# Performance work log

Measured on AMD Instinct MI355X. Metric: run time of the kernel, lower is better.

The kernel has to match this reference:

```python
import jax, jax.numpy as jnp
import numpy as np

N_NODES = 50000
N_EDGES = 800000
D = 128
N_LAYERS = 6  # nbaselayer=3 -> branches of depth 1,2,3
NBASELAYER = 3
BN_EPS = 1e-5


def setup_inputs() -> dict:
    key = jax.random.key(0)
    ks = jax.random.split(key, 11)
    stdv = 1.0 / np.sqrt(D)
    return {
        "x": jax.random.normal(ks[0], (N_NODES, D), jnp.float32),
        "row": jax.random.randint(ks[1], (N_EDGES,), 0, N_NODES),
        "col": jax.random.randint(ks[2], (N_EDGES,), 0, N_NODES),
        "edge_weight": jax.random.uniform(ks[3], (N_EDGES,), jnp.float32),
        "W": jax.random.uniform(ks[4], (N_LAYERS, D, D), jnp.float32, -stdv, stdv),
        "SW": jax.random.uniform(ks[5], (N_LAYERS, D, D), jnp.float32, -stdv, stdv),
        "b": jax.random.uniform(ks[6], (N_LAYERS, D), jnp.float32, -stdv, stdv),
        "gamma": jax.random.uniform(ks[7], (N_LAYERS, D), jnp.float32, 0.5, 1.5),
        "beta": jax.random.normal(ks[8], (N_LAYERS, D), jnp.float32) * 0.1,
        "rmean": jax.random.normal(ks[9], (N_LAYERS, D), jnp.float32) * 0.1,
        "rvar": jax.random.uniform(ks[10], (N_LAYERS, D), jnp.float32, 0.5, 1.5),
    }


def reference(x, row, col, edge_weight, W, SW, b, gamma, beta, rmean, rvar):
    n = x.shape[0]

    def gcn(l, h):
        # dense GEMM: [N, D] @ [D, D]
        support = h @ W[l]
        # sparse aggregation (spmm): out[row] += w * support[col]
        msg = support[col] * edge_weight[:, None]  # [E, D]
        agg = jax.ops.segment_sum(msg, row, num_segments=n)
        # self-loop + bias
        out = agg + h @ SW[l] + b[l]
        # BatchNorm1d (eval mode: running stats)
        out = (out - rmean[l]) * jax.lax.rsqrt(rvar[l] + BN_EPS) * gamma[l] + beta[l]
        return jax.nn.relu(out)

    idx = 0
    for j in range(NBASELAYER):
        subx = x
        for _ in range(j + 1):
            # faithful to source: each inner layer consumes x (not subx)
            subx = gcn(idx, x)
            idx += 1
        x = x + subx  # aggrmethod='add'
    return x
```

## Files before the change

kernel.cpp:

```cpp
#include <hip/hip_runtime.h>

#define DD 128
#define NNODES 50000
#define NEDGES 800000
#define BN_EPS 1e-5f
#define NBLK_SCAN ((NNODES + 255) / 256)
#define NB1 ((NEDGES + 4095) / 4096)
#define NGROUPS ((NNODES + 255) / 256)
#define HIST_BLOCKS ((NEDGES + 255) / 256)

typedef float f32x4 __attribute__((ext_vector_type(4)));
typedef short bf16x8 __attribute__((ext_vector_type(8)));

__device__ __forceinline__ unsigned short f2bf(float f) {
    unsigned u = __float_as_uint(f);
    u = (u + 0x7FFFu + ((u >> 16) & 1u)) >> 16;
    return (unsigned short)u;
}
__device__ __forceinline__ float bf2f(unsigned short s) {
    return __uint_as_float((unsigned)s << 16);
}
__device__ __forceinline__ unsigned packbf(float a, float b) {
    return (unsigned)f2bf(a) | ((unsigned)f2bf(b) << 16);
}
__device__ __forceinline__ float lo_bf(unsigned u) { return __uint_as_float(u << 16); }
__device__ __forceinline__ float hi_bf(unsigned u) { return __uint_as_float(u & 0xFFFF0000u); }

__global__ __launch_bounds__(256) void hist_convx_kernel(
    const int* __restrict__ row, int* __restrict__ deg,
    const float* __restrict__ x, unsigned* __restrict__ h16u,
    int nedges, int npairs)
{
    int bid = blockIdx.x;
    if (bid < HIST_BLOCKS) {
        int e = bid * 256 + threadIdx.x;
        if (e < nedges) atomicAdd(&deg[row[e]], 1);
    } else {
        int stride = (gridDim.x - HIST_BLOCKS) * 256;
        for (int i = (bid - HIST_BLOCKS) * 256 + threadIdx.x; i < npairs; i += stride) {
            float2 v = ((const float2*)x)[i];
            h16u[i] = packbf(v.x, v.y);
        }
    }
}

__global__ __launch_bounds__(256) void scan1_convwf_kernel(
    const int* __restrict__ deg, int* __restrict__ excl, int* __restrict__ bsum,
    const float* __restrict__ W, const float* __restrict__ SW,
    unsigned short* __restrict__ Wf, int n)
{
    if (blockIdx.x >= NBLK_SCAN) {
        int t = (blockIdx.x - NBLK_SCAN) * 256 + threadIdx.x;
        if (t < 3 * 8 * 8 * 64) {
            int lane = t & 63;
            int nt   = (t >> 6) & 7;
            int ks   = (t >> 9) & 7;
            int li   = t >> 12;
            const int lmap[3] = {0, 2, 5};
            int l = lmap[li];
            int nn = nt * 16 + (lane & 15);
            unsigned short* dst = Wf + (((size_t)li * 64 + ks * 8 + nt) * 64 + lane) * 8;
#pragma unroll
            for (int i = 0; i < 8; ++i) {
                int k = ks * 32 + (lane >> 4) * 8 + i;
                float v = (k < 128) ? W[((size_t)l * 128 + k) * 128 + nn]
                                    : SW[((size_t)l * 128 + (k - 128)) * 128 + nn];
                dst[i] = f2bf(v);
            }
        }
        return;
    }
    __shared__ int buf[256];
    int i = blockIdx.x * 256 + threadIdx.x;
    int v = (i < n) ? deg[i] : 0;
    buf[threadIdx.x] = v;
    __syncthreads();
#pragma unroll
    for (int off = 1; off < 256; off <<= 1) {
        int t = (threadIdx.x >= off) ? buf[threadIdx.x - off] : 0;
        __syncthreads();
        buf[threadIdx.x] += t;
        __syncthreads();
    }
    if (i < n) excl[i] = buf[threadIdx.x] - v;
    if (threadIdx.x == 255) bsum[blockIdx.x] = buf[255];
}

__global__ __launch_bounds__(256) void scan2_kernel(
    int* __restrict__ bsum, int* __restrict__ boff, int nblk)
{
    __shared__ int buf[256];
    int v = (threadIdx.x < nblk) ? bsum[threadIdx.x] : 0;
    buf[threadIdx.x] = v;
    __syncthreads();
#pragma unroll
    for (int off = 1; off < 256; off <<= 1) {
        int t = (threadIdx.x >= off) ? buf[threadIdx.x - off] : 0;
        __syncthreads();
        buf[threadIdx.x] += t;
        __syncthreads();
    }
    if (threadIdx.x < nblk) boff[threadIdx.x] = buf[threadIdx.x] - v;
}

__global__ __launch_bounds__(256) void scan3_kernel(
    int* __restrict__ rowptr, const int* __restrict__ boff,
    int* __restrict__ bcur, int n)
{
    int i = blockIdx.x * 256 + threadIdx.x;
    if (i < n) {
        int v = rowptr[i] + boff[blockIdx.x];
        rowptr[i] = v;
        if ((i & 255) == 0) bcur[i >> 8] = v;
    }
    if (i == 0) rowptr[n] = NEDGES;
    if (blockIdx.x == 0 && threadIdx.x >= NGROUPS && threadIdx.x < 256)
        bcur[threadIdx.x] = NEDGES;
}

__global__ __launch_bounds__(256) void sort_pass1_kernel(
    const int* __restrict__ row, const int* __restrict__ col,
    const float* __restrict__ ew, int* __restrict__ bcur,
    uint2* __restrict__ inter, int nedges)
{
    __shared__ int cnt[256];
    __shared__ int base[256];
    cnt[threadIdx.x] = 0;
    __syncthreads();
    const int estart = blockIdx.x * 4096;
    const int eend = min(estart + 4096, nedges);
    for (int e = estart + threadIdx.x; e < eend; e += 256)
        atomicAdd(&cnt[row[e] >> 8], 1);
    __syncthreads();
    base[threadIdx.x] = atomicAdd(&bcur[threadIdx.x], cnt[threadIdx.x]);
    __syncthreads();
    cnt[threadIdx.x] = 0;
    __syncthreads();
    for (int e = estart + threadIdx.x; e < eend; e += 256) {
        int r = row[e];
        int b = r >> 8;
        int k = atomicAdd(&cnt[b], 1);
        unsigned payload = (unsigned)col[e] | ((unsigned)f2bf(ew[e]) << 16);
        inter[base[b] + k] = make_uint2(payload, (unsigned)(r & 255));
    }
}

__global__ __launch_bounds__(256) void sort_pass2_kernel(
    const int* __restrict__ rowptr, const uint2* __restrict__ inter,
    unsigned* __restrict__ cedge, int n)
{
    __shared__ int cur[256];
    const int rows0 = blockIdx.x * 256;
    const int nrows = min(256, n - rows0);
    if (threadIdx.x < nrows) cur[threadIdx.x] = rowptr[rows0 + threadIdx.x];
    __syncthreads();
    const int jbeg = rowptr[rows0];
    const int jend = rowptr[rows0 + nrows];
    for (int j = jbeg + threadIdx.x; j < jend; j += 256) {
        uint2 rec = inter[j];
        int p = atomicAdd(&cur[rec.y], 1);
        cedge[p] = rec.x;
    }
}

__global__ __launch_bounds__(256) void spmm_gather16_kernel(
    const uint2* __restrict__ h2, const int* __restrict__ rowptr,
    const unsigned* __restrict__ ce, uint2* __restrict__ agg2, int n)
{
    int node = blockIdx.x * 4 + (threadIdx.x >> 6);
    if (node >= n) return;
    const int lane = threadIdx.x & 63;
    const int half = lane >> 5;
    const int l32  = lane & 31;
    const int beg = rowptr[node];
    const int end = rowptr[node + 1];

    float a0 = 0.f, a1 = 0.f, a2 = 0.f, a3 = 0.f;
    int j = beg + half;
    for (; j + 6 < end; j += 8) {
        unsigned e0 = ce[j], e1 = ce[j+2], e2 = ce[j+4], e3 = ce[j+6];
        uint2 v0 = h2[(size_t)(e0 & 0xFFFFu) * 32 + l32];
        uint2 v1 = h2[(size_t)(e1 & 0xFFFFu) * 32 + l32];
        uint2 v2 = h2[(size_t)(e2 & 0xFFFFu) * 32 + l32];
        uint2 v3 = h2[(size_t)(e3 & 0xFFFFu) * 32 + l32];
        float w0 = bf2f((unsigned short)(e0 >> 16));
        float w1 = bf2f((unsigned short)(e1 >> 16));
        float w2 = bf2f((unsigned short)(e2 >> 16));
        float w3 = bf2f((unsigned short)(e3 >> 16));
        a0 += w0*lo_bf(v0.x) + w1*lo_bf(v1.x) + w2*lo_bf(v2.x) + w3*lo_bf(v3.x);
        a1 += w0*hi_bf(v0.x) + w1*hi_bf(v1.x) + w2*hi_bf(v2.x) + w3*hi_bf(v3.x);
        a2 += w0*lo_bf(v0.y) + w1*lo_bf(v1.y) + w2*lo_bf(v2.y) + w3*lo_bf(v3.y);
        a3 += w0*hi_bf(v0.y) + w1*hi_bf(v1.y) + w2*hi_bf(v2.y) + w3*hi_bf(v3.y);
    }
    for (; j < end; j += 2) {
        unsigned e = ce[j];
        uint2 v = h2[(size_t)(e & 0xFFFFu) * 32 + l32];
        float w = bf2f((unsigned short)(e >> 16));
        a0 += w * lo_bf(v.x); a1 += w * hi_bf(v.x);
        a2 += w * lo_bf(v.y); a3 += w * hi_bf(v.y);
    }
    a0 += __shfl_xor(a0, 32);
    a1 += __shfl_xor(a1, 32);
    a2 += __shfl_xor(a2, 32);
    a3 += __shfl_xor(a3, 32);
    if (half == 0)
        agg2[(size_t)node * 32 + l32] = make_uint2(packbf(a0, a1), packbf(a2, a3));
}

__global__ __launch_bounds__(256) void gemm_mfma_kernel(
    unsigned short* __restrict__ h16,
    const unsigned short* __restrict__ agg16,
    const unsigned short* __restrict__ Wf,
    const float* __restrict__ bl, const float* __restrict__ gammal,
    const float* __restrict__ betal, const float* __restrict__ rmeanl,
    const float* __restrict__ rvarl,
    float* __restrict__ outf, int n, int write_f32)
{
    __shared__ __align__(16) unsigned short As[64 * 256];
    const int tid  = threadIdx.x;
    const int lane = tid & 63;
    const int wid  = tid >> 6;
    const int brow = blockIdx.x * 64;

    bf16x8 bfr[8][2];
#pragma unroll
    for (int ks = 0; ks < 8; ++ks)
#pragma unroll
        for (int nt2 = 0; nt2 < 2; ++nt2) {
            int nt = wid * 2 + nt2;
            bfr[ks][nt2] = *(const bf16x8*)(Wf + ((size_t)(ks * 8 + nt) * 64 + lane) * 8);
        }

#pragma unroll
    for (int it = 0; it < 8; ++it) {
        int id = tid + it * 256;
        int r  = id >> 5;
        int kc = id & 31;
        int grow = brow + r;
        uint4 v = make_uint4(0, 0, 0, 0);
        if (grow < n) {
            const unsigned short* src = (kc < 16)
                ? (agg16 + (size_t)grow * DD + kc * 8)
                : (h16   + (size_t)grow * DD + (kc - 16) * 8);
            v = *(const uint4*)src;
        }
        int kcs = kc ^ (r & 7);
        *(uint4*)(&As[r * 256 + kcs * 8]) = v;
    }
    __syncthreads();

    f32x4 acc[4][2];
#pragma unroll
    for (int i = 0; i < 4; ++i)
#pragma unroll
        for (int j = 0; j < 2; ++j)
            acc[i][j] = (f32x4){0.f, 0.f, 0.f, 0.f};

#pragma unroll
    for (int ks = 0; ks < 8; ++ks) {
#pragma unroll
        for (int mt = 0; mt < 4; ++mt) {
            int m   = mt * 16 + (lane & 15);
            int kc  = ks * 4 + (lane >> 4);
            int kcs = kc ^ (m & 7);
            bf16x8 afr = *(const bf16x8*)(&As[m * 256 + kcs * 8]);
            acc[mt][0] = __builtin_amdgcn_mfma_f32_16x16x32_bf16(afr, bfr[ks][0], acc[mt][0], 0, 0, 0);
            acc[mt][1] = __builtin_amdgcn_mfma_f32_16x16x32_bf16(afr, bfr[ks][1], acc[mt][1], 0, 0, 0);
        }
    }

#pragma unroll
    for (int nt2 = 0; nt2 < 2; ++nt2) {
        const int gcol = wid * 32 + nt2 * 16 + (lane & 15);
        const float sc = gammal[gcol] * __frsqrt_rn(rvarl[gcol] + BN_EPS);
        const float sh = (bl[gcol] - rmeanl[gcol]) * sc + betal[gcol];
        const int kc_res = 16 + (gcol >> 3);
        const int ko_res = gcol & 7;
#pragma unroll
        for (int mt = 0; mt < 4; ++mt) {
#pragma unroll
            for (int r = 0; r < 4; ++r) {
                int m = mt * 16 + (lane >> 4) * 4 + r;
                int grow = brow + m;
                if (grow < n) {
                    float res = bf2f(As[m * 256 + (kc_res ^ (m & 7)) * 8 + ko_res]);
                    float t = acc[mt][nt2][r] * sc + sh;
                    float o = res + (t > 0.f ? t : 0.f);
                    h16[(size_t)grow * DD + gcol] = f2bf(o);
                    if (write_f32) outf[(size_t)grow * DD + gcol] = o;
                }
            }
        }
    }
}

extern "C" void kernel_launch(void* const* d_in, const int* in_sizes, int n_in,
                              void* d_out, int out_size, void* d_ws, size_t ws_size,
                              hipStream_t stream) {
    const float* x     = (const float*)d_in[0];
    const int*   row   = (const int*)  d_in[1];
    const int*   col   = (const int*)  d_in[2];
    const float* ew    = (const float*)d_in[3];
    const float* W     = (const float*)d_in[4];
    const float* SW    = (const float*)d_in[5];
    const float* b     = (const float*)d_in[6];
    const float* gamma = (const float*)d_in[7];
    const float* beta  = (const float*)d_in[8];
    const float* rmean = (const float*)d_in[9];
    const float* rvar  = (const float*)d_in[10];

    float* out = (float*)d_out;

    char* ws = (char*)d_ws;
    unsigned*       agg16u = (unsigned*)ws;
    unsigned*       h16u   = (unsigned*)(ws + 12800000);
    unsigned short* Wf     = (unsigned short*)(ws + 25600000);
    int*   rowptr = (int*)(ws + 25800000);
    int*   deg    = (int*)(ws + 26010000);
    int*   bsum   = (int*)(ws + 26210016);
    int*   boff   = (int*)(ws + 26211040);
    int*   bcur   = (int*)(ws + 26212064);
    unsigned* cedge = (unsigned*)(ws + 26400000);
    uint2*    inter = (uint2*)(ws + 29600000);

    hipMemsetAsync(deg, 0, NNODES * sizeof(int), stream);
    hist_convx_kernel<<<HIST_BLOCKS + 2048, 256, 0, stream>>>(
        row, deg, x, h16u, NEDGES, NNODES * 64);
    scan1_convwf_kernel<<<NBLK_SCAN + 48, 256, 0, stream>>>(
        deg, rowptr, bsum, W, SW, Wf, NNODES);
    scan2_kernel<<<1, 256, 0, stream>>>(bsum, boff, NBLK_SCAN);
    scan3_kernel<<<NBLK_SCAN, 256, 0, stream>>>(rowptr, boff, bcur, NNODES);
    sort_pass1_kernel<<<NB1, 256, 0, stream>>>(row, col, ew, bcur, inter, NEDGES);
    sort_pass2_kernel<<<NGROUPS, 256, 0, stream>>>(rowptr, inter, cedge, NNODES);

    const int ggrid = (NNODES + 3) / 4;
    const int mgrid = (NNODES + 63) / 64;

    for (int li = 0; li < 3; ++li) {
        const int l = (li == 0) ? 0 : (li == 1) ? 2 : 5;
        spmm_gather16_kernel<<<ggrid, 256, 0, stream>>>(
            (const uint2*)h16u, rowptr, cedge, (uint2*)agg16u, NNODES);
        gemm_mfma_kernel<<<mgrid, 256, 0, stream>>>(
            (unsigned short*)h16u, (const unsigned short*)agg16u,
            Wf + (size_t)li * 32768,
            b + l * DD, gamma + l * DD, beta + l * DD, rmean + l * DD, rvar + l * DD,
            out, NNODES, li == 2 ? 1 : 0);
    }
}
```

Baseline: 226.4 us.

## Restructure CSR build as two-level bucket sort with in-bucket rowptr computation

Replaces the global per-node degree histogram and three-kernel scan with per-block bucket counts, a single-block scan over bucket columns, and per-bucket row-pointer computation inside sort_pass2. This removes the memset, two scan launches and the global atomics on the degree array. It also makes the scatter pass deterministic because it no longer does atomic base allocation. The cost is a serial 196-iteration column scan in one block and an extra read of the intermediate records in pass2.

```diff
diff --git a/kernel.cpp b/kernel.cpp
--- a/kernel.cpp
+++ b/kernel.cpp
@@ -4,10 +4,8 @@
 #define NNODES 50000
 #define NEDGES 800000
 #define BN_EPS 1e-5f
-#define NBLK_SCAN ((NNODES + 255) / 256)
 #define NB1 ((NEDGES + 4095) / 4096)
 #define NGROUPS ((NNODES + 255) / 256)
-#define HIST_BLOCKS ((NEDGES + 255) / 256)
 
 typedef float f32x4 __attribute__((ext_vector_type(4)));
 typedef short bf16x8 __attribute__((ext_vector_type(8)));
@@ -26,116 +24,93 @@
 __device__ __forceinline__ float lo_bf(unsigned u) { return __uint_as_float(u << 16); }
 __device__ __forceinline__ float hi_bf(unsigned u) { return __uint_as_float(u & 0xFFFF0000u); }
 
-__global__ __launch_bounds__(256) void hist_convx_kernel(
-    const int* __restrict__ row, int* __restrict__ deg,
+__global__ __launch_bounds__(256) void count_convx_kernel(
+    const int* __restrict__ row, int* __restrict__ pbase,
     const float* __restrict__ x, unsigned* __restrict__ h16u,
     int nedges, int npairs)
 {
-    int bid = blockIdx.x;
-    if (bid < HIST_BLOCKS) {
-        int e = bid * 256 + threadIdx.x;
-        if (e < nedges) atomicAdd(&deg[row[e]], 1);
+    const int bid = blockIdx.x;
+    if (bid < NB1) {
+        __shared__ int cnt[256];
+        cnt[threadIdx.x] = 0;
+        __syncthreads();
+        const int estart = bid * 4096;
+        const int eend = min(estart + 4096, nedges);
+        for (int e = estart + threadIdx.x; e < eend; e += 256)
+            atomicAdd(&cnt[row[e] >> 8], 1);
+        __syncthreads();
+        pbase[bid * 256 + threadIdx.x] = cnt[threadIdx.x];
     } else {
-        int stride = (gridDim.x - HIST_BLOCKS) * 256;
-        for (int i = (bid - HIST_BLOCKS) * 256 + threadIdx.x; i < npairs; i += stride) {
+        int stride = (gridDim.x - NB1) * 256;
+        for (int i = (bid - NB1) * 256 + threadIdx.x; i < npairs; i += stride) {
             float2 v = ((const float2*)x)[i];
             h16u[i] = packbf(v.x, v.y);
         }
     }
 }
 
-__global__ __launch_bounds__(256) void scan1_convwf_kernel(
-    const int* __restrict__ deg, int* __restrict__ excl, int* __restrict__ bsum,
+__global__ __launch_bounds__(256) void scanall_convwf_kernel(
+    int* __restrict__ pbase, int* __restrict__ bktbase, int* __restrict__ rowptr,
     const float* __restrict__ W, const float* __restrict__ SW,
-    unsigned short* __restrict__ Wf, int n)
-{
-    if (blockIdx.x >= NBLK_SCAN) {
-        int t = (blockIdx.x - NBLK_SCAN) * 256 + threadIdx.x;
-        if (t < 3 * 8 * 8 * 64) {
-            int lane = t & 63;
-            int nt   = (t >> 6) & 7;
-            int ks   = (t >> 9) & 7;
-            int li   = t >> 12;
-            const int lmap[3] = {0, 2, 5};
-            int l = lmap[li];
-            int nn = nt * 16 + (lane & 15);
-            unsigned short* dst = Wf + (((size_t)li * 64 + ks * 8 + nt) * 64 + lane) * 8;
-#pragma unroll
-            for (int i = 0; i < 8; ++i) {
-                int k = ks * 32 + (lane >> 4) * 8 + i;
-                float v = (k < 128) ? W[((size_t)l * 128 + k) * 128 + nn]
-                                    : SW[((size_t)l * 128 + (k - 128)) * 128 + nn];
-                dst[i] = f2bf(v);
-            }
-        }
+    unsigned short* __restrict__ Wf)
+{
+    if (blockIdx.x == 0) {
+        __shared__ int buf[256];
+        const int t = threadIdx.x;
+        int s = 0;
+#pragma unroll 4
+        for (int blk = 0; blk < NB1; ++blk) {
+            int tmp = pbase[blk * 256 + t];
+            pbase[blk * 256 + t] = s;
+            s += tmp;
+        }
+        const int v = s;
+        buf[t] = v;
+        __syncthreads();
+#pragma unroll
+        for (int off = 1; off < 256; off <<= 1) {
+            int tv = (t >= off) ? buf[t - off] : 0;
+            __syncthreads();
+            buf[t] += tv;
+            __syncthreads();
+        }
+        bktbase[t] = buf[t] - v;
+        if (t == 255) bktbase[256] = buf[255];
+        if (t == 0) rowptr[NNODES] = NEDGES;
         return;
     }
-    __shared__ int buf[256];
-    int i = blockIdx.x * 256 + threadIdx.x;
-    int v = (i < n) ? deg[i] : 0;
-    buf[threadIdx.x] = v;
-    __syncthreads();
-#pragma unroll
-    for (int off = 1; off < 256; off <<= 1) {
-        int t = (threadIdx.x >= off) ? buf[threadIdx.x - off] : 0;
-        __syncthreads();
-        buf[threadIdx.x] += t;
-        __syncthreads();
-    }
-    if (i < n) excl[i] = buf[threadIdx.x] - v;
-    if (threadIdx.x == 255) bsum[blockIdx.x] = buf[255];
-}
-
-__global__ __launch_bounds__(256) void scan2_kernel(
-    int* __restrict__ bsum, int* __restrict__ boff, int nblk)
-{
-    __shared__ int buf[256];
-    int v = (threadIdx.x < nblk) ? bsum[threadIdx.x] : 0;
-    buf[threadIdx.x] = v;
-    __syncthreads();
-#pragma unroll
-    for (int off = 1; off < 256; off <<= 1) {
-        int t = (threadIdx.x >= off) ? buf[threadIdx.x - off] : 0;
-        __syncthreads();
-        buf[threadIdx.x] += t;
-        __syncthreads();
-    }
-    if (threadIdx.x < nblk) boff[threadIdx.x] = buf[threadIdx.x] - v;
-}
-
-__global__ __launch_bounds__(256) void scan3_kernel(
-    int* __restrict__ rowptr, const int* __restrict__ boff,
-    int* __restrict__ bcur, int n)
-{
-    int i = blockIdx.x * 256 + threadIdx.x;
-    if (i < n) {
-        int v = rowptr[i] + boff[blockIdx.x];
-        rowptr[i] = v;
-        if ((i & 255) == 0) bcur[i >> 8] = v;
-    }
-    if (i == 0) rowptr[n] = NEDGES;
-    if (blockIdx.x == 0 && threadIdx.x >= NGROUPS && threadIdx.x < 256)
-        bcur[threadIdx.x] = NEDGES;
+    int t = (blockIdx.x - 1) * 256 + threadIdx.x;
+    if (t < 3 * 8 * 8 * 64) {
+        int lane = t & 63;
+        int nt   = (t >> 6) & 7;
+        int ks   = (t >> 9) & 7;
+        int li   = t >> 12;
+        const int lmap[3] = {0, 2, 5};
+        int l = lmap[li];
+        int nn = nt * 16 + (lane & 15);
+        unsigned short* dst = Wf + (((size_t)li * 64 + ks * 8 + nt) * 64 + lane) * 8;
+#pragma unroll
+        for (int i = 0; i < 8; ++i) {
+            int k = ks * 32 + (lane >> 4) * 8 + i;
+            float v = (k < 128) ? W[((size_t)l * 128 + k) * 128 + nn]
+                                : SW[((size_t)l * 128 + (k - 128)) * 128 + nn];
+            dst[i] = f2bf(v);
+        }
+    }
 }
 
 __global__ __launch_bounds__(256) void sort_pass1_kernel(
     const int* __restrict__ row, const int* __restrict__ col,
-    const float* __restrict__ ew, int* __restrict__ bcur,
-    uint2* __restrict__ inter, int nedges)
-{
+    const float* __restrict__ ew, const int* __restrict__ pbase,
+    const int* __restrict__ bktbase, uint2* __restrict__ inter, int nedges)
+{
+    __shared__ int base[256];
     __shared__ int cnt[256];
-    __shared__ int base[256];
+    base[threadIdx.x] = pbase[blockIdx.x * 256 + threadIdx.x] + bktbase[threadIdx.x];
     cnt[threadIdx.x] = 0;
     __syncthreads();
     const int estart = blockIdx.x * 4096;
     const int eend = min(estart + 4096, nedges);
-    for (int e = estart + threadIdx.x; e < eend; e += 256)
-        atomicAdd(&cnt[row[e] >> 8], 1);
-    __syncthreads();
-    base[threadIdx.x] = atomicAdd(&bcur[threadIdx.x], cnt[threadIdx.x]);
-    __syncthreads();
-    cnt[threadIdx.x] = 0;
-    __syncthreads();
     for (int e = estart + threadIdx.x; e < eend; e += 256) {
         int r = row[e];
         int b = r >> 8;
@@ -146,16 +121,33 @@
 }
 
 __global__ __launch_bounds__(256) void sort_pass2_kernel(
-    const int* __restrict__ rowptr, const uint2* __restrict__ inter,
-    unsigned* __restrict__ cedge, int n)
-{
+    const int* __restrict__ bktbase, const uint2* __restrict__ inter,
+    int* __restrict__ rowptr, unsigned* __restrict__ cedge, int n)
+{
+    __shared__ int cnt[256];
     __shared__ int cur[256];
-    const int rows0 = blockIdx.x * 256;
-    const int nrows = min(256, n - rows0);
-    if (threadIdx.x < nrows) cur[threadIdx.x] = rowptr[rows0 + threadIdx.x];
-    __syncthreads();
-    const int jbeg = rowptr[rows0];
-    const int jend = rowptr[rows0 + nrows];
+    const int g = blockIdx.x;
+    const int rows0 = g * 256;
+    const int jbeg = bktbase[g];
+    const int jend = bktbase[g + 1];
+    cnt[threadIdx.x] = 0;
+    __syncthreads();
+    for (int j = jbeg + threadIdx.x; j < jend; j += 256)
+        atomicAdd(&cnt[inter[j].y], 1);
+    __syncthreads();
+    const int v = cnt[threadIdx.x];
+    __syncthreads();
+#pragma unroll
+    for (int off = 1; off < 256; off <<= 1) {
+        int t = (threadIdx.x >= off) ? cnt[threadIdx.x - off] : 0;
+        __syncthreads();
+        cnt[threadIdx.x] += t;
+        __syncthreads();
+    }
+    const int rp = jbeg + cnt[threadIdx.x] - v;
+    if (rows0 + threadIdx.x < n) rowptr[rows0 + threadIdx.x] = rp;
+    cur[threadIdx.x] = rp;
+    __syncthreads();
     for (int j = jbeg + threadIdx.x; j < jend; j += 256) {
         uint2 rec = inter[j];
         int p = atomicAdd(&cur[rec.y], 1);
@@ -315,23 +307,20 @@
     unsigned*       agg16u = (unsigned*)ws;
     unsigned*       h16u   = (unsigned*)(ws + 12800000);
     unsigned short* Wf     = (unsigned short*)(ws + 25600000);
-    int*   rowptr = (int*)(ws + 25800000);
-    int*   deg    = (int*)(ws + 26010000);
-    int*   bsum   = (int*)(ws + 26210016);
-    int*   boff   = (int*)(ws + 26211040);
-    int*   bcur   = (int*)(ws + 26212064);
+    int*   rowptr  = (int*)(ws + 25800000);
+    int*   pbase   = (int*)(ws + 26010000);
+    int*   bktbase = (int*)(ws + 26220000);
     unsigned* cedge = (unsigned*)(ws + 26400000);
     uint2*    inter = (uint2*)(ws + 29600000);
 
-    hipMemsetAsync(deg, 0, NNODES * sizeof(int), stream);
-    hist_convx_kernel<<<HIST_BLOCKS + 2048, 256, 0, stream>>>(
-        row, deg, x, h16u, NEDGES, NNODES * 64);
-    scan1_convwf_kernel<<<NBLK_SCAN + 48, 256, 0, stream>>>(
-        deg, rowptr, bsum, W, SW, Wf, NNODES);
-    scan2_kernel<<<1, 256, 0, stream>>>(bsum, boff, NBLK_SCAN);
-    scan3_kernel<<<NBLK_SCAN, 256, 0, stream>>>(rowptr, boff, bcur, NNODES);
-    sort_pass1_kernel<<<NB1, 256, 0, stream>>>(row, col, ew, bcur, inter, NEDGES);
-    sort_pass2_kernel<<<NGROUPS, 256, 0, stream>>>(rowptr, inter, cedge, NNODES);
+    count_convx_kernel<<<NB1 + 2048, 256, 0, stream>>>(
+        row, pbase, x, h16u, NEDGES, NNODES * 64);
+    scanall_convwf_kernel<<<1 + 48, 256, 0, stream>>>(
+        pbase, bktbase, rowptr, W, SW, Wf);
+    sort_pass1_kernel<<<NB1, 256, 0, stream>>>(
+        row, col, ew, pbase, bktbase, inter, NEDGES);
+    sort_pass2_kernel<<<NGROUPS, 256, 0, stream>>>(
+        bktbase, inter, rowptr, cedge, NNODES);
 
     const int ggrid = (NNODES + 3) / 4;
     const int mgrid = (NNODES + 63) / 64;
```

After: 194.4 us. 14.1% less time.
